# Kernel tuning notes

Measured on AMD Instinct MI355X. Metric: run time of the kernel, lower is better.

The kernel has to match this reference:

```python
import jax, jax.numpy as jnp
import numpy as np

B, S, D_IN, D_OUT = 4, 2048, 1024, 1024

def setup_inputs() -> dict:
    key = jax.random.key(0)
    k0, k1, k2, k3 = jax.random.split(key, 4)
    sc = 1.0 / np.sqrt(D_IN)
    return {
        "x": jax.random.normal(k0, (B, S, D_IN), dtype=jnp.float32),
        "wq": jax.random.normal(k1, (D_OUT, D_IN), dtype=jnp.float32) * sc,
        "wk": jax.random.normal(k2, (D_OUT, D_IN), dtype=jnp.float32) * sc,
        "wv": jax.random.normal(k3, (D_OUT, D_IN), dtype=jnp.float32) * sc,
    }

def reference(x, wq, wk, wv):
    # Linear (no bias): y = x @ W.T, W shaped [d_out, d_in]
    q = jnp.einsum("bsd,ed->bse", x, wq)
    k = jnp.einsum("bsd,ed->bse", x, wk)
    v = jnp.einsum("bsd,ed->bse", x, wv)
    scores = jnp.einsum("bqe,bke->bqk", q, k)  # [B,S,S]
    n = x.shape[1]
    causal = jnp.triu(jnp.ones((n, n), dtype=bool), k=1)  # True above diagonal -> masked
    scores = jnp.where(causal, -jnp.inf, scores)
    attn = jax.nn.softmax(scores / jnp.sqrt(jnp.asarray(k.shape[-1], scores.dtype)), axis=-1)
    # dropout p=0.0 -> identity
    return jnp.einsum("bqk,bke->bqe", attn, v)
```

## Files before the change

### kernel.cpp

```cpp
#include <hip/hip_runtime.h>

#define Bb 4
#define Ss 2048
#define Dd 1024

typedef unsigned short u16;
typedef __bf16 bf16x8 __attribute__((ext_vector_type(8)));
typedef float  f32x4  __attribute__((ext_vector_type(4)));

__device__ inline u16 f2bf(float f) {
  union { float f; unsigned u; } x; x.f = f;
  unsigned u = x.u;
  return (u16)((u + 0x7fffu + ((u >> 16) & 1u)) >> 16);
}
__device__ inline float bf2f(u16 h) {
  union { unsigned u; float f; } x; x.u = ((unsigned)h) << 16;
  return x.f;
}

__device__ static inline void gl_lds16(const u16* g, u16* l) {
  __builtin_amdgcn_global_load_lds((__attribute__((address_space(1))) const void*)g,
                                   (__attribute__((address_space(3))) void*)l,
                                   16, 0, 0);
}

__global__ __launch_bounds__(256) void cast_all(const float* __restrict__ x,
                                                const float* __restrict__ wq,
                                                const float* __restrict__ wk,
                                                const float* __restrict__ wv,
                                                u16* __restrict__ xb,
                                                u16* __restrict__ wb) {
  int id = blockIdx.x;
  const float* src; u16* dst; int off;
  if (id < 8192) {
    src = x; dst = xb; off = id * 1024;
  } else {
    int wi = id - 8192;
    int w = wi >> 10;
    src = (w == 0) ? wq : (w == 1) ? wk : wv;
    dst = wb + (size_t)w * Dd * Dd;
    off = (wi & 1023) * 1024;
  }
  int i = off + threadIdx.x * 4;
  float4 v = *(const float4*)(src + i);
  unsigned p0 = (unsigned)f2bf(v.x) | ((unsigned)f2bf(v.y) << 16);
  unsigned p1 = (unsigned)f2bf(v.z) | ((unsigned)f2bf(v.w) << 16);
  uint2 p; p.x = p0; p.y = p1;
  *(uint2*)(dst + i) = p;
}

#define BM 128
#define BN 128
#define BK 32

__device__ inline void gemm_tile(const u16* __restrict__ A, int lda,
                                 const u16* __restrict__ Bp, int ldb,
                                 int kBeg, int kEnd,
                                 u16* lA, u16* lB, f32x4 acc[4][4]) {
  const int tid  = threadIdx.x;
  const int lane = tid & 63, wave = tid >> 6;
  const int quad = lane >> 4, r16 = lane & 15;
  const int wm = (wave & 1) * 64, wn = (wave >> 1) * 64;

  for (int k0 = kBeg; k0 < kEnd; k0 += BK) {
    __syncthreads();
#pragma unroll
    for (int q = 0; q < 2; q++) {
      int s = q * 256 + tid;
      int row = s >> 2, part = s & 3;
      gl_lds16(A + (size_t)row * lda + k0 + part * 8, lA + s * 8);
    }
#pragma unroll
    for (int q = 0; q < 2; q++) {
      int s = q * 256 + tid;
      int row = s >> 2, part = s & 3;
      gl_lds16(Bp + (size_t)row * ldb + k0 + part * 8, lB + s * 8);
    }
    __syncthreads();
    bf16x8 fa[4], fb[4];
#pragma unroll
    for (int t = 0; t < 4; t++)
      fa[t] = *(const bf16x8*)(lA + (wm + t * 16 + r16) * 32 + quad * 8);
#pragma unroll
    for (int t = 0; t < 4; t++)
      fb[t] = *(const bf16x8*)(lB + (wn + t * 16 + r16) * 32 + quad * 8);
#pragma unroll
    for (int tm = 0; tm < 4; tm++)
#pragma unroll
      for (int tn = 0; tn < 4; tn++)
        acc[tm][tn] = __builtin_amdgcn_mfma_f32_16x16x32_bf16(fa[tm], fb[tn],
                                                              acc[tm][tn], 0, 0, 0);
  }
}

__global__ __launch_bounds__(256) void qkv_gemm(const u16* __restrict__ xb,
                                                const u16* __restrict__ wb,
                                                u16* __restrict__ qkv) {
  __shared__ __align__(16) u16 shmem[8192];
  u16* lA = shmem;
  u16* lB = shmem + 4096;
  const int id  = blockIdx.x;
  const int xcd = id & 7, j = id >> 3;
  const int xt  = j & 7;
  const int yl  = (j >> 3) & 7;
  const int zi  = j >> 6;
  const int y   = xcd * 8 + yl;
  const int row0 = y * BM;
  const int col0 = xt * BN;
  const u16* A  = xb + (size_t)row0 * Dd;
  const u16* Bp = wb + (size_t)zi * Dd * Dd + (size_t)col0 * Dd;
  f32x4 acc[4][4];
  const f32x4 zero = {0.f, 0.f, 0.f, 0.f};
#pragma unroll
  for (int tm = 0; tm < 4; tm++)
#pragma unroll
    for (int tn = 0; tn < 4; tn++) acc[tm][tn] = zero;

  gemm_tile(A, Dd, Bp, Dd, 0, Dd, lA, lB, acc);

  u16* out = qkv + (size_t)zi * ((size_t)Bb * Ss * Dd);
  const int lane = threadIdx.x & 63, wave = threadIdx.x >> 6;
  const int quad = lane >> 4, r16 = lane & 15;
  const int wm = (wave & 1) * 64, wn = (wave >> 1) * 64;
#pragma unroll
  for (int tm = 0; tm < 4; tm++)
#pragma unroll
    for (int tn = 0; tn < 4; tn++) {
      int rr = row0 + wm + tm * 16 + quad * 4;
      int cc = col0 + wn + tn * 16 + r16;
#pragma unroll
      for (int r = 0; r < 4; r++)
        out[(size_t)(rr + r) * Dd + cc] = f2bf(acc[tm][tn][r]);
    }
}

__global__ __launch_bounds__(256) void scores_fused(const u16* __restrict__ qb,
                                                    const u16* __restrict__ kb,
                                                    const u16* __restrict__ vb,
                                                    u16* __restrict__ sc,
                                                    u16* __restrict__ vt,
                                                    float* __restrict__ lsum) {
  __shared__ __align__(16) u16 shmem[8192];
  const int id = blockIdx.x;
  const int tid = threadIdx.x;

  if (id >= 544) {
    const int t2 = id - 544;
    const int b = t2 >> 7, rem = t2 & 127;
    const int e = rem >> 3, g = rem & 7;
    const u16* src = vb + (size_t)b * Ss * Dd;
    u16* dst = vt + (size_t)b * Dd * Ss;
    u16 (*t)[72] = (u16(*)[72])shmem;
    for (int q4 = 0; q4 < 4; q4++) {
      int s0 = (g * 4 + q4) * 64, e0 = e * 64;
      if (q4) __syncthreads();
#pragma unroll
      for (int gg = tid; gg < 512; gg += 256) {
        int row = gg >> 3, part = gg & 7;
        uint4 v = *(const uint4*)(src + (size_t)(s0 + row) * Dd + e0 + part * 8);
        const u16* pv = (const u16*)&v;
#pragma unroll
        for (int jj = 0; jj < 8; jj++) t[part * 8 + jj][row] = pv[jj];
      }
      __syncthreads();
#pragma unroll
      for (int gg = tid; gg < 512; gg += 256) {
        int ee = gg >> 3, part = gg & 7;
        uint4 v = *(const uint4*)(&t[ee][part * 8]);
        *(uint4*)(dst + (size_t)(e0 + ee) * Ss + s0 + part * 8) = v;
      }
    }
    return;
  }

  const int xcd = id & 7, j = id >> 3;
  const int b = j / 17, tloc = j - b * 17;
  const int t = xcd * 17 + tloc;
  int it = (int)((sqrtf(8.f * (float)t + 1.f) - 1.f) * 0.5f);
  while ((it + 1) * (it + 2) / 2 <= t) it++;
  while (it * (it + 1) / 2 > t) it--;
  const int jt = t - it * (it + 1) / 2;

  u16* lA = shmem;
  u16* lB = shmem + 4096;
  const u16* A  = qb + (size_t)b * Ss * Dd + (size_t)it * BM * Dd;
  const u16* Bp = kb + (size_t)b * Ss * Dd + (size_t)jt * BN * Dd;
  f32x4 acc[4][4];
  const f32x4 zero = {0.f, 0.f, 0.f, 0.f};
#pragma unroll
  for (int tm = 0; tm < 4; tm++)
#pragma unroll
    for (int tn = 0; tn < 4; tn++) acc[tm][tn] = zero;

  gemm_tile(A, Dd, Bp, Dd, 0, Dd, lA, lB, acc);

  u16* out = sc + (size_t)b * Ss * Ss;
  float* lr = lsum + (size_t)b * Ss;
  const int lane = tid & 63, wave = tid >> 6;
  const int quad = lane >> 4, r16 = lane & 15;
  const int wm = (wave & 1) * 64, wn = (wave >> 1) * 64;
#pragma unroll
  for (int tm = 0; tm < 4; tm++) {
    float psum[4] = {0.f, 0.f, 0.f, 0.f};
#pragma unroll
    for (int tn = 0; tn < 4; tn++) {
      int rr = it * BM + wm + tm * 16 + quad * 4;
      int cc = jt * BN + wn + tn * 16 + r16;
#pragma unroll
      for (int r = 0; r < 4; r++) {
        float p = 0.f;
        u16 h = 0;
        if (cc <= rr + r) {
          h = f2bf(__expf(acc[tm][tn][r] * 0.03125f));
          p = bf2f(h);
        }
        out[(size_t)(rr + r) * Ss + cc] = h;
        psum[r] += p;
      }
    }
#pragma unroll
    for (int r = 0; r < 4; r++) {
      float s = psum[r];
      s += __shfl_xor(s, 1);
      s += __shfl_xor(s, 2);
      s += __shfl_xor(s, 4);
      s += __shfl_xor(s, 8);
      if (r16 == 0) {
        int row = it * BM + wm + tm * 16 + quad * 4 + r;
        atomicAdd(&lr[row], s);
      }
    }
  }
}

__global__ __launch_bounds__(256) void pv_gemm(const u16* __restrict__ sc,
                                               const u16* __restrict__ vt,
                                               const float* __restrict__ lsum,
                                               float* __restrict__ out) {
  __shared__ __align__(16) u16 shmem[8192];
  u16* lA = shmem;
  u16* lB = shmem + 4096;
  const int idx = blockIdx.x;
  const int it = 15 - (idx >> 5);
  const int rem = idx & 31;
  const int col0 = (rem & 7) * BN;
  const int b = rem >> 3;
  const int row0 = it * BM;
  const u16* A  = sc + (size_t)b * Ss * Ss + (size_t)row0 * Ss;
  const u16* Bp = vt + (size_t)b * Dd * Ss + (size_t)col0 * Ss;
  f32x4 acc[4][4];
  const f32x4 zero = {0.f, 0.f, 0.f, 0.f};
#pragma unroll
  for (int tm = 0; tm < 4; tm++)
#pragma unroll
    for (int tn = 0; tn < 4; tn++) acc[tm][tn] = zero;

  gemm_tile(A, Ss, Bp, Ss, 0, row0 + BM, lA, lB, acc);

  float* o = out + (size_t)b * Ss * Dd;
  const float* lr = lsum + (size_t)b * Ss;
  const int lane = threadIdx.x & 63, wave = threadIdx.x >> 6;
  const int quad = lane >> 4, r16 = lane & 15;
  const int wm = (wave & 1) * 64, wn = (wave >> 1) * 64;
#pragma unroll
  for (int tm = 0; tm < 4; tm++) {
    int rbase = row0 + wm + tm * 16 + quad * 4;
    float s0 = 1.f / lr[rbase], s1 = 1.f / lr[rbase + 1];
    float s2 = 1.f / lr[rbase + 2], s3 = 1.f / lr[rbase + 3];
#pragma unroll
    for (int tn = 0; tn < 4; tn++) {
      int cc = col0 + wn + tn * 16 + r16;
      o[(size_t)(rbase + 0) * Dd + cc] = acc[tm][tn][0] * s0;
      o[(size_t)(rbase + 1) * Dd + cc] = acc[tm][tn][1] * s1;
      o[(size_t)(rbase + 2) * Dd + cc] = acc[tm][tn][2] * s2;
      o[(size_t)(rbase + 3) * Dd + cc] = acc[tm][tn][3] * s3;
    }
  }
}

extern "C" void kernel_launch(void* const* d_in, const int* in_sizes, int n_in,
                              void* d_out, int out_size, void* d_ws, size_t ws_size,
                              hipStream_t stream) {
  const float* x  = (const float*)d_in[0];
  const float* wq = (const float*)d_in[1];
  const float* wk = (const float*)d_in[2];
  const float* wv = (const float*)d_in[3];
  float* out = (float*)d_out;
  char* ws = (char*)d_ws;
  if (ws_size < 106987520u) return;

  u16* qkv  = (u16*)(ws);
  u16* sc   = (u16*)(ws + 50331648u);
  u16* xb   = (u16*)(ws + 83886080u);
  u16* vt   = xb;
  u16* wb   = (u16*)(ws + 100663296u);
  float* lsum = (float*)(ws + 106954752u);

  const size_t nQ = (size_t)Bb * Ss * Dd;

  hipMemsetAsync(lsum, 0, Bb * Ss * sizeof(float), stream);
  cast_all<<<11264, 256, 0, stream>>>(x, wq, wk, wv, xb, wb);
  qkv_gemm<<<1536, 256, 0, stream>>>(xb, wb, qkv);
  scores_fused<<<1056, 256, 0, stream>>>(qkv, qkv + nQ, qkv + 2 * nQ, sc, vt, lsum);
  pv_gemm<<<512, 256, 0, stream>>>(sc, vt, lsum, out);
}
```

Baseline: 239.4 us.

## Deepen GEMM K-step, fold memset into cast, rebalance transpose and PV order

The shared GEMM tile now loads 64 K-elements per iteration into two LDS halves, which halves the number of barrier pairs per tile at the cost of doubling LDS per block. The lsum memset is folded into the cast kernel, and each cast block now converts four chunks instead of one. The V transpose blocks become a grid-stride loop over 480 blocks, so scores_fused launches fewer blocks. pv_gemm interleaves long and short row tiles to balance the causal workload. The larger LDS footprint may reduce occupancy.

```diff
diff --git a/kernel.cpp b/kernel.cpp
--- a/kernel.cpp
+++ b/kernel.cpp
@@ -29,76 +29,90 @@
                                                 const float* __restrict__ wk,
                                                 const float* __restrict__ wv,
                                                 u16* __restrict__ xb,
-                                                u16* __restrict__ wb) {
+                                                u16* __restrict__ wb,
+                                                float* __restrict__ lsum) {
   int id = blockIdx.x;
+  if (id < 8) {
+    float4 z = {0.f, 0.f, 0.f, 0.f};
+    ((float4*)lsum)[id * 256 + threadIdx.x] = z;
+  }
   const float* src; u16* dst; int off;
-  if (id < 8192) {
-    src = x; dst = xb; off = id * 1024;
+  if (id < 2048) {
+    src = x; dst = xb; off = id * 4096;
   } else {
-    int wi = id - 8192;
-    int w = wi >> 10;
+    int wi = id - 2048;
+    int w = wi >> 8;
     src = (w == 0) ? wq : (w == 1) ? wk : wv;
     dst = wb + (size_t)w * Dd * Dd;
-    off = (wi & 1023) * 1024;
-  }
-  int i = off + threadIdx.x * 4;
-  float4 v = *(const float4*)(src + i);
-  unsigned p0 = (unsigned)f2bf(v.x) | ((unsigned)f2bf(v.y) << 16);
-  unsigned p1 = (unsigned)f2bf(v.z) | ((unsigned)f2bf(v.w) << 16);
-  uint2 p; p.x = p0; p.y = p1;
-  *(uint2*)(dst + i) = p;
+    off = (wi & 255) * 4096;
+  }
+#pragma unroll
+  for (int t = 0; t < 4; t++) {
+    int i = off + t * 1024 + threadIdx.x * 4;
+    float4 v = *(const float4*)(src + i);
+    unsigned p0 = (unsigned)f2bf(v.x) | ((unsigned)f2bf(v.y) << 16);
+    unsigned p1 = (unsigned)f2bf(v.z) | ((unsigned)f2bf(v.w) << 16);
+    uint2 p; p.x = p0; p.y = p1;
+    *(uint2*)(dst + i) = p;
+  }
 }
 
 #define BM 128
 #define BN 128
-#define BK 32
 
 __device__ inline void gemm_tile(const u16* __restrict__ A, int lda,
                                  const u16* __restrict__ Bp, int ldb,
                                  int kBeg, int kEnd,
-                                 u16* lA, u16* lB, f32x4 acc[4][4]) {
+                                 u16* lds, f32x4 acc[4][4]) {
+  u16* lA0 = lds;
+  u16* lB0 = lds + 4096;
+  u16* lA1 = lds + 8192;
+  u16* lB1 = lds + 12288;
   const int tid  = threadIdx.x;
   const int lane = tid & 63, wave = tid >> 6;
   const int quad = lane >> 4, r16 = lane & 15;
   const int wm = (wave & 1) * 64, wn = (wave >> 1) * 64;
-
-  for (int k0 = kBeg; k0 < kEnd; k0 += BK) {
+  const int r0 = tid >> 2, part = tid & 3;
+
+  for (int k0 = kBeg; k0 < kEnd; k0 += 64) {
     __syncthreads();
 #pragma unroll
     for (int q = 0; q < 2; q++) {
-      int s = q * 256 + tid;
-      int row = s >> 2, part = s & 3;
-      gl_lds16(A + (size_t)row * lda + k0 + part * 8, lA + s * 8);
-    }
-#pragma unroll
-    for (int q = 0; q < 2; q++) {
-      int s = q * 256 + tid;
-      int row = s >> 2, part = s & 3;
-      gl_lds16(Bp + (size_t)row * ldb + k0 + part * 8, lB + s * 8);
+      int row = q * 64 + r0;
+      int s8 = (q * 256 + tid) * 8;
+      const u16* ga = A  + (size_t)row * lda + k0 + part * 8;
+      const u16* gb = Bp + (size_t)row * ldb + k0 + part * 8;
+      gl_lds16(ga,      lA0 + s8);
+      gl_lds16(gb,      lB0 + s8);
+      gl_lds16(ga + 32, lA1 + s8);
+      gl_lds16(gb + 32, lB1 + s8);
     }
     __syncthreads();
-    bf16x8 fa[4], fb[4];
-#pragma unroll
-    for (int t = 0; t < 4; t++)
-      fa[t] = *(const bf16x8*)(lA + (wm + t * 16 + r16) * 32 + quad * 8);
-#pragma unroll
-    for (int t = 0; t < 4; t++)
-      fb[t] = *(const bf16x8*)(lB + (wn + t * 16 + r16) * 32 + quad * 8);
-#pragma unroll
-    for (int tm = 0; tm < 4; tm++)
-#pragma unroll
-      for (int tn = 0; tn < 4; tn++)
-        acc[tm][tn] = __builtin_amdgcn_mfma_f32_16x16x32_bf16(fa[tm], fb[tn],
-                                                              acc[tm][tn], 0, 0, 0);
+#pragma unroll
+    for (int h = 0; h < 2; h++) {
+      const u16* la = h ? lA1 : lA0;
+      const u16* lb = h ? lB1 : lB0;
+      bf16x8 fa[4], fb[4];
+#pragma unroll
+      for (int t = 0; t < 4; t++)
+        fa[t] = *(const bf16x8*)(la + (wm + t * 16 + r16) * 32 + quad * 8);
+#pragma unroll
+      for (int t = 0; t < 4; t++)
+        fb[t] = *(const bf16x8*)(lb + (wn + t * 16 + r16) * 32 + quad * 8);
+#pragma unroll
+      for (int tm = 0; tm < 4; tm++)
+#pragma unroll
+        for (int tn = 0; tn < 4; tn++)
+          acc[tm][tn] = __builtin_amdgcn_mfma_f32_16x16x32_bf16(fa[tm], fb[tn],
+                                                                acc[tm][tn], 0, 0, 0);
+    }
   }
 }
 
 __global__ __launch_bounds__(256) void qkv_gemm(const u16* __restrict__ xb,
                                                 const u16* __restrict__ wb,
                                                 u16* __restrict__ qkv) {
-  __shared__ __align__(16) u16 shmem[8192];
-  u16* lA = shmem;
-  u16* lB = shmem + 4096;
+  __shared__ __align__(16) u16 shmem[16384];
   const int id  = blockIdx.x;
   const int xcd = id & 7, j = id >> 3;
   const int xt  = j & 7;
@@ -116,7 +130,7 @@
 #pragma unroll
     for (int tn = 0; tn < 4; tn++) acc[tm][tn] = zero;
 
-  gemm_tile(A, Dd, Bp, Dd, 0, Dd, lA, lB, acc);
+  gemm_tile(A, Dd, Bp, Dd, 0, Dd, shmem, acc);
 
   u16* out = qkv + (size_t)zi * ((size_t)Bb * Ss * Dd);
   const int lane = threadIdx.x & 63, wave = threadIdx.x >> 6;
@@ -140,34 +154,33 @@
                                                     u16* __restrict__ sc,
                                                     u16* __restrict__ vt,
                                                     float* __restrict__ lsum) {
-  __shared__ __align__(16) u16 shmem[8192];
+  __shared__ __align__(16) u16 shmem[16384];
   const int id = blockIdx.x;
   const int tid = threadIdx.x;
 
   if (id >= 544) {
-    const int t2 = id - 544;
-    const int b = t2 >> 7, rem = t2 & 127;
-    const int e = rem >> 3, g = rem & 7;
-    const u16* src = vb + (size_t)b * Ss * Dd;
-    u16* dst = vt + (size_t)b * Dd * Ss;
+    const int bid = id - 544;
     u16 (*t)[72] = (u16(*)[72])shmem;
-    for (int q4 = 0; q4 < 4; q4++) {
-      int s0 = (g * 4 + q4) * 64, e0 = e * 64;
-      if (q4) __syncthreads();
+    for (int u = bid; u < 2048; u += 480) {
+      const int b = u >> 9, rem = u & 511;
+      const int e0 = (rem >> 5) * 64, s0 = (rem & 31) * 64;
+      const u16* src = vb + (size_t)b * Ss * Dd;
+      u16* dst = vt + (size_t)b * Dd * Ss;
+      if (u != bid) __syncthreads();
 #pragma unroll
       for (int gg = tid; gg < 512; gg += 256) {
-        int row = gg >> 3, part = gg & 7;
-        uint4 v = *(const uint4*)(src + (size_t)(s0 + row) * Dd + e0 + part * 8);
+        int row = gg >> 3, prt = gg & 7;
+        uint4 v = *(const uint4*)(src + (size_t)(s0 + row) * Dd + e0 + prt * 8);
         const u16* pv = (const u16*)&v;
 #pragma unroll
-        for (int jj = 0; jj < 8; jj++) t[part * 8 + jj][row] = pv[jj];
+        for (int jj = 0; jj < 8; jj++) t[prt * 8 + jj][row] = pv[jj];
       }
       __syncthreads();
 #pragma unroll
       for (int gg = tid; gg < 512; gg += 256) {
-        int ee = gg >> 3, part = gg & 7;
-        uint4 v = *(const uint4*)(&t[ee][part * 8]);
-        *(uint4*)(dst + (size_t)(e0 + ee) * Ss + s0 + part * 8) = v;
+        int ee = gg >> 3, prt = gg & 7;
+        uint4 v = *(const uint4*)(&t[ee][prt * 8]);
+        *(uint4*)(dst + (size_t)(e0 + ee) * Ss + s0 + prt * 8) = v;
       }
     }
     return;
@@ -181,8 +194,6 @@
   while (it * (it + 1) / 2 > t) it--;
   const int jt = t - it * (it + 1) / 2;
 
-  u16* lA = shmem;
-  u16* lB = shmem + 4096;
   const u16* A  = qb + (size_t)b * Ss * Dd + (size_t)it * BM * Dd;
   const u16* Bp = kb + (size_t)b * Ss * Dd + (size_t)jt * BN * Dd;
   f32x4 acc[4][4];
@@ -192,7 +203,7 @@
 #pragma unroll
     for (int tn = 0; tn < 4; tn++) acc[tm][tn] = zero;
 
-  gemm_tile(A, Dd, Bp, Dd, 0, Dd, lA, lB, acc);
+  gemm_tile(A, Dd, Bp, Dd, 0, Dd, shmem, acc);
 
   u16* out = sc + (size_t)b * Ss * Ss;
   float* lr = lsum + (size_t)b * Ss;
@@ -237,11 +248,10 @@
                                                const u16* __restrict__ vt,
                                                const float* __restrict__ lsum,
                                                float* __restrict__ out) {
-  __shared__ __align__(16) u16 shmem[8192];
-  u16* lA = shmem;
-  u16* lB = shmem + 4096;
+  __shared__ __align__(16) u16 shmem[16384];
   const int idx = blockIdx.x;
-  const int it = 15 - (idx >> 5);
+  const int slot = idx >> 5;
+  const int it = (slot < 8) ? (15 - 2 * slot) : (2 * (slot - 8));
   const int rem = idx & 31;
   const int col0 = (rem & 7) * BN;
   const int b = rem >> 3;
@@ -255,7 +265,7 @@
 #pragma unroll
     for (int tn = 0; tn < 4; tn++) acc[tm][tn] = zero;
 
-  gemm_tile(A, Ss, Bp, Ss, 0, row0 + BM, lA, lB, acc);
+  gemm_tile(A, Ss, Bp, Ss, 0, row0 + BM, shmem, acc);
 
   float* o = out + (size_t)b * Ss * Dd;
   const float* lr = lsum + (size_t)b * Ss;
@@ -298,9 +308,8 @@
 
   const size_t nQ = (size_t)Bb * Ss * Dd;
 
-  hipMemsetAsync(lsum, 0, Bb * Ss * sizeof(float), stream);
-  cast_all<<<11264, 256, 0, stream>>>(x, wq, wk, wv, xb, wb);
+  cast_all<<<2816, 256, 0, stream>>>(x, wq, wk, wv, xb, wb, lsum);
   qkv_gemm<<<1536, 256, 0, stream>>>(xb, wb, qkv);
-  scores_fused<<<1056, 256, 0, stream>>>(qkv, qkv + nQ, qkv + 2 * nQ, sc, vt, lsum);
+  scores_fused<<<1024, 256, 0, stream>>>(qkv, qkv + nQ, qkv + 2 * nQ, sc, vt, lsum);
   pv_gemm<<<512, 256, 0, stream>>>(sc, vt, lsum, out);
 }
```

Measured after the change: 237.3 us. No clear change (-0.9%).
